# Performance work log

Hardware: AMD Instinct MI355X
Metric: run time of the kernel (lower is better)

Reference implementation:

```python
import jax, jax.numpy as jnp
import numpy as np

KERNEL_LAM = 0.003


def setup_inputs() -> dict:
    key = jax.random.key(0)
    ks = jax.random.split(key, 5)
    B, H, L, Lk = 2, 2048, 4096, 128
    u = jax.random.normal(ks[0], (B, H, L), dtype=jnp.float32)
    kernel = jax.random.normal(ks[1], (1, H, Lk), dtype=jnp.float32) * 0.002
    D = jax.random.normal(ks[2], (1, H), dtype=jnp.float32)
    W_out = jax.random.normal(ks[3], (2 * H, H), dtype=jnp.float32) / np.sqrt(H)
    b_out = jnp.zeros((2 * H,), dtype=jnp.float32)
    return {"u": u, "kernel": kernel, "D": D, "W_out": W_out, "b_out": b_out}


def reference(u, kernel, D, W_out, b_out):
    # u: [B, H, L]; kernel: [C=1, H, Lk]; D: [C, H]; W_out: [2H, H]; b_out: [2H]
    B, H, L = u.shape
    n = 2 * L
    # soft-threshold kernel
    k = jax.nn.relu(jnp.abs(kernel) - KERNEL_LAM) * jnp.sign(kernel)
    k_f = jnp.fft.rfft(k, n=n)            # [C, H, L+1] complex
    u_f = jnp.fft.rfft(u, n=n)            # [B, H, L+1] complex
    y_f = jnp.einsum('bhl,chl->bchl', u_f, k_f)
    y = jnp.fft.irfft(y_f, n=n)[..., :L]  # [B, C, H, L]
    y = y + jnp.einsum('bhl,ch->bchl', u, D)
    y = y.reshape(B, -1, L)               # [B, C*H, L]
    y = jax.nn.gelu(y, approximate=False)
    # output_linear: 1x1 conv H -> 2H, then GLU over channel dim
    y = jnp.einsum('oh,bhl->bol', W_out, y) + b_out[None, :, None]
    a, g = jnp.split(y, 2, axis=1)
    return a * jax.nn.sigmoid(g)          # [B, H, L]
```

## Files before the change

### kernel.cpp

```cpp
#include <hip/hip_runtime.h>
#include <stdint.h>

typedef short short8 __attribute__((ext_vector_type(8)));
typedef float f32x4 __attribute__((ext_vector_type(4)));

#define KLAM 0.003f

__device__ __forceinline__ uint16_t f2bf(float f) {
  union { float f; uint32_t u; } v; v.f = f;
  uint32_t r = v.u + 0x7fffu + ((v.u >> 16) & 1u);
  return (uint16_t)(r >> 16);
}
__device__ __forceinline__ uint32_t pack_lo(uint32_t a, uint32_t b) { return (a & 0xffffu) | (b << 16); }
__device__ __forceinline__ uint32_t pack_hi(uint32_t a, uint32_t b) { return (a >> 16) | (b & 0xffff0000u); }
__device__ __forceinline__ int swzB(int n) { return ((n & 7) ^ ((n >> 3) & 7)); }

typedef __attribute__((address_space(3))) uint32_t* lds_u32p;
typedef const __attribute__((address_space(1))) uint32_t* gbl_u32p;
__device__ __forceinline__ void gload16(const void* g, void* l) {
  __builtin_amdgcn_global_load_lds((gbl_u32p)g, (lds_u32p)l, 16, 0, 0);
}

__global__ __launch_bounds__(256) void cast_w_kernel(const float* __restrict__ W,
                                                     uint16_t* __restrict__ Wb) {
  int i = (blockIdx.x * 256 + threadIdx.x) * 8;
  float4 f0 = *(const float4*)(W + i);
  float4 f1 = *(const float4*)(W + i + 4);
  uint4 q;
  q.x = (uint32_t)f2bf(f0.x) | ((uint32_t)f2bf(f0.y) << 16);
  q.y = (uint32_t)f2bf(f0.z) | ((uint32_t)f2bf(f0.w) << 16);
  q.z = (uint32_t)f2bf(f1.x) | ((uint32_t)f2bf(f1.y) << 16);
  q.w = (uint32_t)f2bf(f1.z) | ((uint32_t)f2bf(f1.w) << 16);
  *(uint4*)(Wb + i) = q;
}

__global__ __launch_bounds__(256) void conv_gelu_kernel(const float* __restrict__ u,
                                                        const float* __restrict__ kern,
                                                        const float* __restrict__ D,
                                                        uint16_t* __restrict__ X) {
  __shared__ __align__(16) float su[4096];
  __shared__ __align__(16) uint16_t ubf[4256];
  __shared__ __align__(16) uint16_t kR[176];
  __shared__ __align__(16) uint16_t stg[4][256];

  int tid = threadIdx.x;
  int bh = blockIdx.x;
  int h = bh & 2047;
  int b = bh >> 11;
  int lane = tid & 63;
  int wv = tid >> 6;
  int ln15 = lane & 15;
  int g = lane >> 4;

  const float4* u4 = (const float4*)(u + (size_t)bh * 4096);
#pragma unroll
  for (int i = 0; i < 4; ++i) {
    float4 v = u4[i * 256 + tid];
    ((float4*)su)[i * 256 + tid] = v;
    uint2 p;
    p.x = (uint32_t)f2bf(v.x) | ((uint32_t)f2bf(v.y) << 16);
    p.y = (uint32_t)f2bf(v.z) | ((uint32_t)f2bf(v.w) << 16);
    *(uint2*)(ubf + 160 + (i * 256 + tid) * 4) = p;
  }
  if (tid < 40) { uint2 z; z.x = 0; z.y = 0; *(uint2*)(ubf + tid * 4) = z; }
  if (tid < 176) {
    int i = 159 - tid;
    uint16_t r = 0;
    if (i >= 0 && i < 128) {
      float kv = kern[h * 128 + i];
      float a = fabsf(kv) - KLAM;
      float s = (a > 0.f) ? (kv > 0.f ? a : -a) : 0.f;
      r = f2bf(s);
    }
    kR[tid] = r;
  }
  __syncthreads();

  float Dh = D[h];

  short8 bfr[5];
#pragma unroll
  for (int q = 0; q < 5; ++q) {
    int z0 = 143 - 32 * q - ln15 + 8 * g;
    union { short8 v; uint16_t s[8]; } t;
#pragma unroll
    for (int e = 0; e < 8; ++e) t.s[e] = kR[z0 + e];
    bfr[q] = t.v;
  }

#pragma unroll
  for (int it = 0; it < 4; ++it) {
    int T0 = (wv * 4 + it) * 256;
    f32x4 acc = {0.f, 0.f, 0.f, 0.f};
#pragma unroll
    for (int q = 0; q < 5; ++q) {
      const short8 a = *(const short8*)(ubf + 160 + T0 + 16 * ln15 - 16 - 32 * q + 8 * g);
      acc = __builtin_amdgcn_mfma_f32_16x16x32_bf16(a, bfr[q], acc, 0, 0, 0);
    }
#pragma unroll
    for (int r = 0; r < 4; ++r) {
      int m = 4 * g + r;
      int t = T0 + 16 * m + ln15;
      float y = acc[r] + Dh * su[t];
      float ge = 0.5f * y * (1.f + erff(y * 0.70710678118654752f));
      stg[wv][16 * m + ln15] = f2bf(ge);
    }
    uint2 v = *(uint2*)(&stg[wv][lane * 4]);
    *(uint2*)(X + (size_t)h * 8192 + (size_t)b * 4096 + T0 + lane * 4) = v;
  }
}

__global__ __launch_bounds__(256) void transpose_kernel(const uint16_t* __restrict__ X,
                                                        uint16_t* __restrict__ XT) {
  __shared__ uint16_t t[64][66];
  int tid = threadIdx.x;
  int bn = blockIdx.x & 127;
  int bk = blockIdx.x >> 7;
  int n0 = bn << 6, k0 = bk << 6;
  int cr = tid >> 3;
  int cc = (tid & 7) * 8;
#pragma unroll
  for (int p = 0; p < 2; ++p) {
    int kr = p * 32 + cr;
    uint4 v = *(const uint4*)(X + (size_t)(k0 + kr) * 8192 + n0 + cc);
    const uint16_t* s = (const uint16_t*)&v;
#pragma unroll
    for (int e = 0; e < 8; ++e) t[cc + e][kr] = s[e];
  }
  __syncthreads();
#pragma unroll
  for (int p = 0; p < 2; ++p) {
    int nl = p * 32 + cr;
    uint16_t d[8];
#pragma unroll
    for (int e = 0; e < 8; ++e) d[e] = t[nl][cc + e];
    *(uint4*)(XT + (size_t)(n0 + nl) * 2048 + k0 + cc) = *(uint4*)d;
  }
}

__global__ __launch_bounds__(512, 2) void gemm_glu_v9(const uint16_t* __restrict__ Wb,
                                                      const uint16_t* __restrict__ XT,
                                                      const float* __restrict__ bout,
                                                      float* __restrict__ out) {
  __shared__ __align__(16) char lds[131072];

  int tid = threadIdx.x;
  int lane = tid & 63;
  int wv = tid >> 6;
  int wr = wv >> 2;
  int wc = wv & 3;
  int ln15 = lane & 15;
  int g16 = lane >> 4;

  int bid = blockIdx.x;
  int xcd = bid & 7, idx = bid >> 3;
  int bn = xcd * 4 + (idx & 3);
  int bm = idx >> 2;
  int mo0 = bm * 128, n0 = bn * 256;

  int lr8 = lane >> 3;
  int sb = (((lane & 7) ^ lr8) << 4);
  const char* pAA = (const char*)Wb + (size_t)(mo0 + wv * 16 + lr8) * 4096 + sb;
  const char* pAG = (const char*)Wb + (size_t)(2048 + mo0 + wv * 16 + lr8) * 4096 + sb;
  const char* pBL = (const char*)XT + (size_t)(n0 + wv * 16 + lr8) * 4096 + sb;
  const char* pBH = (const char*)XT + (size_t)(n0 + 128 + wv * 16 + lr8) * 4096 + sb;
  uint32_t ldW = wv * 2048;

  auto stAA = [&](int buf, const char* p) {
    char* d = lds + buf * 32768 + ldW;
    gload16(p, d); gload16(p + 32768, d + 1024);
  };
  auto stAG = [&](int buf, const char* p) {
    char* d = lds + buf * 32768 + 16384 + ldW;
    gload16(p, d); gload16(p + 32768, d + 1024);
  };
  auto stBL = [&](int buf, const char* p) {
    char* d = lds + 65536 + buf * 32768 + ldW;
    gload16(p, d); gload16(p + 32768, d + 1024);
  };
  auto stBH = [&](int buf, const char* p) {
    char* d = lds + 65536 + buf * 32768 + 16384 + ldW;
    gload16(p, d); gload16(p + 32768, d + 1024);
  };

  int sw = (ln15 & 7) << 4;
  uint32_t aoff0 = (uint32_t)((wr * 64 + ln15) * 128 + ((g16 * 16) ^ sw));
  uint32_t aoff1 = (uint32_t)((wr * 64 + ln15) * 128 + ((64 + g16 * 16) ^ sw));
  uint32_t boff0 = (uint32_t)(65536 + (wc * 64 + ln15) * 128 + ((g16 * 16) ^ sw));
  uint32_t boff1 = (uint32_t)(65536 + (wc * 64 + ln15) * 128 + ((64 + g16 * 16) ^ sw));

  f32x4 zero = {0.f, 0.f, 0.f, 0.f};
  f32x4 acc_a[4][4], acc_g[4][4];
#pragma unroll
  for (int mi = 0; mi < 4; ++mi)
#pragma unroll
    for (int ni = 0; ni < 4; ++ni) { acc_a[mi][ni] = zero; acc_g[mi][ni] = zero; }

  short8 fa[4][2], fg[4][2], fb[4][2];

  stAA(0, pAA); stBL(0, pBL); stAG(0, pAG); stBH(0, pBH);
  stAA(1, pAA + 128); stBL(1, pBL + 128); stAG(1, pAG + 128);
  pAA += 256; pBL += 256; pAG += 256; pBH += 128;
  asm volatile("s_waitcnt vmcnt(6)" ::: "memory");
  __builtin_amdgcn_s_barrier();

  auto KTILE = [&](int t, int cur) {
#pragma unroll
    for (int mi = 0; mi < 4; ++mi) {
      fa[mi][0] = *(const short8*)(lds + cur * 32768 + mi * 2048 + aoff0);
      fa[mi][1] = *(const short8*)(lds + cur * 32768 + mi * 2048 + aoff1);
    }
#pragma unroll
    for (int ni = 0; ni < 2; ++ni) {
      fb[ni][0] = *(const short8*)(lds + cur * 32768 + ni * 2048 + boff0);
      fb[ni][1] = *(const short8*)(lds + cur * 32768 + ni * 2048 + boff1);
    }
    if (t < 31) stBH(cur ^ 1, pBH);
    __builtin_amdgcn_s_barrier();
    __builtin_amdgcn_s_setprio(1);
#pragma unroll
    for (int mi = 0; mi < 4; ++mi)
#pragma unroll
      for (int ni = 0; ni < 2; ++ni)
#pragma unroll
        for (int kk = 0; kk < 2; ++kk)
          acc_a[mi][ni] = __builtin_amdgcn_mfma_f32_16x16x32_bf16(fa[mi][kk], fb[ni][kk], acc_a[mi][ni], 0, 0, 0);
    __builtin_amdgcn_s_setprio(0);
    __builtin_amdgcn_s_barrier();

#pragma unroll
    for (int ni = 2; ni < 4; ++ni) {
      fb[ni][0] = *(const short8*)(lds + cur * 32768 + ni * 2048 + boff0);
      fb[ni][1] = *(const short8*)(lds + cur * 32768 + ni * 2048 + boff1);
    }
    if (t < 30) stAA(cur, pAA);
    __builtin_amdgcn_s_barrier();
    __builtin_amdgcn_s_setprio(1);
#pragma unroll
    for (int mi = 0; mi < 4; ++mi)
#pragma unroll
      for (int ni = 2; ni < 4; ++ni)
#pragma unroll
        for (int kk = 0; kk < 2; ++kk)
          acc_a[mi][ni] = __builtin_amdgcn_mfma_f32_16x16x32_bf16(fa[mi][kk], fb[ni][kk], acc_a[mi][ni], 0, 0, 0);
    __builtin_amdgcn_s_setprio(0);
    __builtin_amdgcn_s_barrier();

#pragma unroll
    for (int mi = 0; mi < 4; ++mi) {
      fg[mi][0] = *(const short8*)(lds + cur * 32768 + 16384 + mi * 2048 + aoff0);
      fg[mi][1] = *(const short8*)(lds + cur * 32768 + 16384 + mi * 2048 + aoff1);
    }
    if (t < 30) stBL(cur, pBL);
    __builtin_amdgcn_s_barrier();
    __builtin_amdgcn_s_setprio(1);
#pragma unroll
    for (int mi = 0; mi < 4; ++mi)
#pragma unroll
      for (int ni = 0; ni < 2; ++ni)
#pragma unroll
        for (int kk = 0; kk < 2; ++kk)
          acc_g[mi][ni] = __builtin_amdgcn_mfma_f32_16x16x32_bf16(fg[mi][kk], fb[ni][kk], acc_g[mi][ni], 0, 0, 0);
    __builtin_amdgcn_s_setprio(0);
    __builtin_amdgcn_s_barrier();

    if (t < 30) {
      stAG(cur, pAG);
      asm volatile("s_waitcnt vmcnt(6)" ::: "memory");
    } else {
      asm volatile("s_waitcnt vmcnt(0)" ::: "memory");
    }
    __builtin_amdgcn_s_barrier();
    __builtin_amdgcn_s_setprio(1);
#pragma unroll
    for (int mi = 0; mi < 4; ++mi)
#pragma unroll
      for (int ni = 2; ni < 4; ++ni)
#pragma unroll
        for (int kk = 0; kk < 2; ++kk)
          acc_g[mi][ni] = __builtin_amdgcn_mfma_f32_16x16x32_bf16(fg[mi][kk], fb[ni][kk], acc_g[mi][ni], 0, 0, 0);
    __builtin_amdgcn_s_setprio(0);
    __builtin_amdgcn_s_barrier();

    pAA += 128; pBL += 128; pAG += 128; pBH += 128;
  };

  for (int tt = 0; tt < 16; ++tt) {
    KTILE(2 * tt, 0);
    KTILE(2 * tt + 1, 1);
  }

#pragma unroll
  for (int mi = 0; mi < 4; ++mi) {
    int ob = mo0 + wr * 64 + mi * 16 + g16 * 4;
    float4 ba4 = *(const float4*)(bout + ob);
    float4 bg4 = *(const float4*)(bout + ob + 2048);
    const float* bap = (const float*)&ba4;
    const float* bgp = (const float*)&bg4;
#pragma unroll
    for (int q = 0; q < 4; ++q) {
      int o = ob + q;
#pragma unroll
      for (int ni = 0; ni < 4; ++ni) {
        float av = acc_a[mi][ni][q] + bap[q];
        float gv = acc_g[mi][ni][q] + bgp[q];
        float res = av / (1.f + expf(-gv));
        int n = n0 + wc * 64 + ni * 16 + ln15;
        out[(size_t)(n >> 12) * 8388608 + (size_t)o * 4096 + (n & 4095)] = res;
      }
    }
  }
}

__global__ __launch_bounds__(256, 2) void gemm_glu_v1(const uint16_t* __restrict__ Wb,
                                                      const uint16_t* __restrict__ X,
                                                      const float* __restrict__ bout,
                                                      float* __restrict__ out) {
  __shared__ char lds[65536];

  int tid = threadIdx.x;
  int lane = tid & 63;
  int wv = tid >> 6;

  int bid = blockIdx.x;
  int wg = (bid & 7) * 256 + (bid >> 3);
  int bm = wg >> 6, bn = wg & 63;
  int m0 = bm * 64, n0 = bn * 128;

  int arb = tid >> 3;
  int ab = (tid & 7) * 16;
  const char* Aglob[4];
  uint32_t AwAddr[4];
#pragma unroll
  for (int i = 0; i < 4; ++i) {
    int r = i * 32 + arb;
    int o = (r < 64) ? (m0 + r) : (2048 + m0 + (r - 64));
    Aglob[i] = (const char*)Wb + (size_t)o * 4096 + ab;
    AwAddr[i] = (uint32_t)(r * 128 + (ab ^ ((r & 7) << 4)));
  }
  int n4 = (tid & 31) * 4;
  int kg = (tid >> 5) * 8;
  const char* Bglob = (const char*)X + ((size_t)kg * 8192 + (size_t)(n0 + n4)) * 2;
  uint32_t BwAddr[4];
#pragma unroll
  for (int no = 0; no < 4; ++no) {
    int n = n4 + no;
    BwAddr[no] = (uint32_t)(n * 128 + (((tid >> 5) * 16) ^ (swzB(n) << 4)));
  }

  f32x4 zero = {0.f, 0.f, 0.f, 0.f};
  f32x4 acc_a[2][4], acc_g[2][4];
#pragma unroll
  for (int mi = 0; mi < 2; ++mi)
#pragma unroll
    for (int ni = 0; ni < 4; ++ni) { acc_a[mi][ni] = zero; acc_g[mi][ni] = zero; }

  uint4 aR[4];
  uint2 bR[8];
  auto LOAD = [&](int t) {
    size_t koff = (size_t)t * 128;
#pragma unroll
    for (int i = 0; i < 4; ++i) aR[i] = *(const uint4*)(Aglob[i] + koff);
    size_t bko = (size_t)t * 64 * 16384;
#pragma unroll
    for (int i = 0; i < 8; ++i) bR[i] = *(const uint2*)(Bglob + bko + (size_t)i * 16384);
  };
  auto WRITE = [&](int buf) {
    char* A = lds + buf * 16384;
#pragma unroll
    for (int i = 0; i < 4; ++i) *(uint4*)(A + AwAddr[i]) = aR[i];
    char* Bb = lds + 32768 + buf * 16384;
    {
      uint4 q; q.x = pack_lo(bR[0].x, bR[1].x); q.y = pack_lo(bR[2].x, bR[3].x);
      q.z = pack_lo(bR[4].x, bR[5].x); q.w = pack_lo(bR[6].x, bR[7].x);
      *(uint4*)(Bb + BwAddr[0]) = q;
    }
    {
      uint4 q; q.x = pack_hi(bR[0].x, bR[1].x); q.y = pack_hi(bR[2].x, bR[3].x);
      q.z = pack_hi(bR[4].x, bR[5].x); q.w = pack_hi(bR[6].x, bR[7].x);
      *(uint4*)(Bb + BwAddr[1]) = q;
    }
    {
      uint4 q; q.x = pack_lo(bR[0].y, bR[1].y); q.y = pack_lo(bR[2].y, bR[3].y);
      q.z = pack_lo(bR[4].y, bR[5].y); q.w = pack_lo(bR[6].y, bR[7].y);
      *(uint4*)(Bb + BwAddr[2]) = q;
    }
    {
      uint4 q; q.x = pack_hi(bR[0].y, bR[1].y); q.y = pack_hi(bR[2].y, bR[3].y);
      q.z = pack_hi(bR[4].y, bR[5].y); q.w = pack_hi(bR[6].y, bR[7].y);
      *(uint4*)(Bb + BwAddr[3]) = q;
    }
  };

  LOAD(0);
  WRITE(0);
  __syncthreads();

  for (int t = 0; t < 32; ++t) {
    int cur = t & 1;
    if (t < 31) LOAD(t + 1);

    const char* A = lds + cur * 16384;
    const char* Bb = lds + 32768 + cur * 16384;
#pragma unroll
    for (int kk = 0; kk < 2; ++kk) {
      int kbyte = kk * 64 + ((lane >> 4) << 4);
      short8 fa[2], fg[2], fb[4];
#pragma unroll
      for (int mi = 0; mi < 2; ++mi) {
        int ra = (wv >> 1) * 32 + mi * 16 + (lane & 15);
        fa[mi] = *(const short8*)(A + ra * 128 + (kbyte ^ ((ra & 7) << 4)));
        int rg = 64 + ra;
        fg[mi] = *(const short8*)(A + rg * 128 + (kbyte ^ ((rg & 7) << 4)));
      }
#pragma unroll
      for (int ni = 0; ni < 4; ++ni) {
        int n = (wv & 1) * 64 + ni * 16 + (lane & 15);
        fb[ni] = *(const short8*)(Bb + n * 128 + (kbyte ^ (swzB(n) << 4)));
      }
#pragma unroll
      for (int mi = 0; mi < 2; ++mi)
#pragma unroll
        for (int ni = 0; ni < 4; ++ni) {
          acc_a[mi][ni] = __builtin_amdgcn_mfma_f32_16x16x32_bf16(fa[mi], fb[ni], acc_a[mi][ni], 0, 0, 0);
          acc_g[mi][ni] = __builtin_amdgcn_mfma_f32_16x16x32_bf16(fg[mi], fb[ni], acc_g[mi][ni], 0, 0, 0);
        }
    }

    if (t < 31) WRITE(cur ^ 1);
    __syncthreads();
  }

  int colb = n0 + (wv & 1) * 64;
#pragma unroll
  for (int mi = 0; mi < 2; ++mi) {
    int ob = m0 + (wv >> 1) * 32 + mi * 16 + ((lane >> 4) << 2);
#pragma unroll
    for (int q = 0; q < 4; ++q) {
      int o = ob + q;
      float ba = bout[o];
      float bg = bout[o + 2048];
#pragma unroll
      for (int ni = 0; ni < 4; ++ni) {
        float av = acc_a[mi][ni][q] + ba;
        float gv = acc_g[mi][ni][q] + bg;
        float res = av / (1.f + expf(-gv));
        int n = colb + ni * 16 + (lane & 15);
        out[(size_t)(n >> 12) * 8388608 + (size_t)o * 4096 + (n & 4095)] = res;
      }
    }
  }
}

extern "C" void kernel_launch(void* const* d_in, const int* in_sizes, int n_in,
                              void* d_out, int out_size, void* d_ws, size_t ws_size,
                              hipStream_t stream) {
  const float* u    = (const float*)d_in[0];
  const float* kern = (const float*)d_in[1];
  const float* D    = (const float*)d_in[2];
  const float* W    = (const float*)d_in[3];
  const float* bo   = (const float*)d_in[4];
  float* out = (float*)d_out;

  uint16_t* Wb = (uint16_t*)d_ws;
  uint16_t* X  = (uint16_t*)((char*)d_ws + (size_t)16 * 1024 * 1024);
  uint16_t* XT = (uint16_t*)((char*)d_ws + (size_t)48 * 1024 * 1024);

  hipLaunchKernelGGL(cast_w_kernel,    dim3(4096), dim3(256), 0, stream, W, Wb);
  hipLaunchKernelGGL(conv_gelu_kernel, dim3(4096), dim3(256), 0, stream, u, kern, D, X);
  if (ws_size >= (size_t)80 * 1024 * 1024) {
    hipLaunchKernelGGL(transpose_kernel, dim3(4096), dim3(256), 0, stream, X, XT);
    hipLaunchKernelGGL(gemm_glu_v9,      dim3(512),  dim3(512), 0, stream, Wb, XT, bo, out);
  } else {
    hipLaunchKernelGGL(gemm_glu_v1,      dim3(2048), dim3(256), 0, stream, Wb, X, bo, out);
  }
}
```

Measured before the change: 178.2 us.

## Merge GEMM k-tile phases from four to two with reordered LDS staging

Restructures the inner k-tile loop of the GLU GEMM from four barrier-separated MFMA phases to two. Each phase now loads all B fragments and does the full a or g accumulation. The global-to-LDS staging is rescheduled: the gate A tile for the next buffer is prefetched alongside the B high half, and the A and B low stores are issued together, with adjusted vmcnt waits. The aim is fewer barriers per k-tile and larger MFMA bursts, at the cost of more live fragment registers and a changed overlap between loads and compute.

```diff
diff --git a/kernel.cpp b/kernel.cpp
--- a/kernel.cpp
+++ b/kernel.cpp
@@ -138,10 +138,10 @@
   }
 }
 
-__global__ __launch_bounds__(512, 2) void gemm_glu_v9(const uint16_t* __restrict__ Wb,
-                                                      const uint16_t* __restrict__ XT,
-                                                      const float* __restrict__ bout,
-                                                      float* __restrict__ out) {
+__global__ __launch_bounds__(512, 2) void gemm_glu_v10(const uint16_t* __restrict__ Wb,
+                                                       const uint16_t* __restrict__ XT,
+                                                       const float* __restrict__ bout,
+                                                       float* __restrict__ out) {
   __shared__ __align__(16) char lds[131072];
 
   int tid = threadIdx.x;
@@ -199,9 +199,9 @@
   short8 fa[4][2], fg[4][2], fb[4][2];
 
   stAA(0, pAA); stBL(0, pBL); stAG(0, pAG); stBH(0, pBH);
-  stAA(1, pAA + 128); stBL(1, pBL + 128); stAG(1, pAG + 128);
-  pAA += 256; pBL += 256; pAG += 256; pBH += 128;
-  asm volatile("s_waitcnt vmcnt(6)" ::: "memory");
+  stAA(1, pAA + 128); stBL(1, pBL + 128);
+  pAA += 256; pBL += 256; pAG += 128; pBH += 128;
+  asm volatile("s_waitcnt vmcnt(4)" ::: "memory");
   __builtin_amdgcn_s_barrier();
 
   auto KTILE = [&](int t, int cur) {
@@ -211,17 +211,17 @@
       fa[mi][1] = *(const short8*)(lds + cur * 32768 + mi * 2048 + aoff1);
     }
 #pragma unroll
-    for (int ni = 0; ni < 2; ++ni) {
+    for (int ni = 0; ni < 4; ++ni) {
       fb[ni][0] = *(const short8*)(lds + cur * 32768 + ni * 2048 + boff0);
       fb[ni][1] = *(const short8*)(lds + cur * 32768 + ni * 2048 + boff1);
     }
-    if (t < 31) stBH(cur ^ 1, pBH);
+    if (t < 31) { stBH(cur ^ 1, pBH); stAG(cur ^ 1, pAG); }
     __builtin_amdgcn_s_barrier();
     __builtin_amdgcn_s_setprio(1);
 #pragma unroll
     for (int mi = 0; mi < 4; ++mi)
 #pragma unroll
-      for (int ni = 0; ni < 2; ++ni)
+      for (int ni = 0; ni < 4; ++ni)
 #pragma unroll
         for (int kk = 0; kk < 2; ++kk)
           acc_a[mi][ni] = __builtin_amdgcn_mfma_f32_16x16x32_bf16(fa[mi][kk], fb[ni][kk], acc_a[mi][ni], 0, 0, 0);
@@ -229,53 +229,22 @@
     __builtin_amdgcn_s_barrier();
 
 #pragma unroll
-    for (int ni = 2; ni < 4; ++ni) {
-      fb[ni][0] = *(const short8*)(lds + cur * 32768 + ni * 2048 + boff0);
-      fb[ni][1] = *(const short8*)(lds + cur * 32768 + ni * 2048 + boff1);
-    }
-    if (t < 30) stAA(cur, pAA);
-    __builtin_amdgcn_s_barrier();
-    __builtin_amdgcn_s_setprio(1);
-#pragma unroll
-    for (int mi = 0; mi < 4; ++mi)
-#pragma unroll
-      for (int ni = 2; ni < 4; ++ni)
-#pragma unroll
-        for (int kk = 0; kk < 2; ++kk)
-          acc_a[mi][ni] = __builtin_amdgcn_mfma_f32_16x16x32_bf16(fa[mi][kk], fb[ni][kk], acc_a[mi][ni], 0, 0, 0);
-    __builtin_amdgcn_s_setprio(0);
-    __builtin_amdgcn_s_barrier();
-
-#pragma unroll
     for (int mi = 0; mi < 4; ++mi) {
       fg[mi][0] = *(const short8*)(lds + cur * 32768 + 16384 + mi * 2048 + aoff0);
       fg[mi][1] = *(const short8*)(lds + cur * 32768 + 16384 + mi * 2048 + aoff1);
     }
-    if (t < 30) stBL(cur, pBL);
+    if (t < 30) {
+      stAA(cur, pAA); stBL(cur, pBL);
+      asm volatile("s_waitcnt vmcnt(4)" ::: "memory");
+    } else {
+      asm volatile("s_waitcnt vmcnt(0)" ::: "memory");
+    }
     __builtin_amdgcn_s_barrier();
     __builtin_amdgcn_s_setprio(1);
 #pragma unroll
     for (int mi = 0; mi < 4; ++mi)
 #pragma unroll
-      for (int ni = 0; ni < 2; ++ni)
-#pragma unroll
-        for (int kk = 0; kk < 2; ++kk)
-          acc_g[mi][ni] = __builtin_amdgcn_mfma_f32_16x16x32_bf16(fg[mi][kk], fb[ni][kk], acc_g[mi][ni], 0, 0, 0);
-    __builtin_amdgcn_s_setprio(0);
-    __builtin_amdgcn_s_barrier();
-
-    if (t < 30) {
-      stAG(cur, pAG);
-      asm volatile("s_waitcnt vmcnt(6)" ::: "memory");
-    } else {
-      asm volatile("s_waitcnt vmcnt(0)" ::: "memory");
-    }
-    __builtin_amdgcn_s_barrier();
-    __builtin_amdgcn_s_setprio(1);
-#pragma unroll
-    for (int mi = 0; mi < 4; ++mi)
-#pragma unroll
-      for (int ni = 2; ni < 4; ++ni)
+      for (int ni = 0; ni < 4; ++ni)
 #pragma unroll
         for (int kk = 0; kk < 2; ++kk)
           acc_g[mi][ni] = __builtin_amdgcn_mfma_f32_16x16x32_bf16(fg[mi][kk], fb[ni][kk], acc_g[mi][ni], 0, 0, 0);
@@ -470,7 +439,7 @@
   hipLaunchKernelGGL(conv_gelu_kernel, dim3(4096), dim3(256), 0, stream, u, kern, D, X);
   if (ws_size >= (size_t)80 * 1024 * 1024) {
     hipLaunchKernelGGL(transpose_kernel, dim3(4096), dim3(256), 0, stream, X, XT);
-    hipLaunchKernelGGL(gemm_glu_v9,      dim3(512),  dim3(512), 0, stream, Wb, XT, bo, out);
+    hipLaunchKernelGGL(gemm_glu_v10,     dim3(512),  dim3(512), 0, stream, Wb, XT, bo, out);
   } else {
     hipLaunchKernelGGL(gemm_glu_v1,      dim3(2048), dim3(256), 0, stream, Wb, X, bo, out);
   }
```

Result: faster. 170.2 us (-4.5%).
